# Performance work log

Hardware: AMD Instinct MI355X
Metric: run time of the kernel (lower is better)

## Reference

```python
import jax, jax.numpy as jnp
import numpy as np

S = 41          # seq_len
D_IN = 1280
D_OUT = 1024
HEADS = 4
HC = D_OUT // HEADS
EPS = 1e-5

# ---- static edge construction (faithful to the torch code, incl. duplicate edges) ----

def _local_edges(s, window=1):
    e = []
    for i in range(s):
        for j in range(max(0, i - window), min(s, i + window + 1)):
            if i != j:
                e += [(i, j), (j, i)]
    return np.array(e, dtype=np.int32).T

def _region_edges(s):
    e = []
    step = s // 3
    for st in range(0, s, step):
        blk = range(st, min(st + step, s))
        for i in blk:
            for j in blk:
                if i != j:
                    e += [(i, j), (j, i)]
    return np.array(e, dtype=np.int32).T

def _global_edges(s):
    r, c = np.triu_indices(s, 1)  # torch.combinations: (i, j) with i < j
    return np.stack([r, c]).astype(np.int32)

def _batch_edges(e, b, s):
    off = np.arange(b, dtype=np.int32) * s
    return (e[:, None, :] + off[None, :, None]).reshape(2, -1)

_LOCAL = _local_edges(S)
_REGION = _region_edges(S)
_GLOBAL = _global_edges(S)

# ---- layer primitives ----

def _layernorm(x, g, b):
    mu = x.mean(-1, keepdims=True)
    v = ((x - mu) ** 2).mean(-1, keepdims=True)
    return (x - mu) / jnp.sqrt(v + EPS) * g + b

def _gcn(x, w, b, src, tgt, n):
    # PyG GCNConv: x' = D^-1/2 (A + I) D^-1/2 (x W) + b
    h = x @ w
    sl = jnp.arange(n, dtype=src.dtype)
    s = jnp.concatenate([src, sl]); t = jnp.concatenate([tgt, sl])
    deg = jax.ops.segment_sum(jnp.ones(t.shape, h.dtype), t, n)
    dinv = jnp.where(deg > 0, jax.lax.rsqrt(jnp.maximum(deg, 1.0)), 0.0)
    norm = dinv[s] * dinv[t]
    return jax.ops.segment_sum(h[s] * norm[:, None], t, n) + b

def _gat(x, w, a_src, a_dst, b, src, tgt, n):
    # PyG GATConv (shared lin, self loops, leaky_relu 0.2, softmax over incoming edges)
    h = (x @ w).reshape(n, HEADS, HC)
    sl = jnp.arange(n, dtype=src.dtype)
    s = jnp.concatenate([src, sl]); t = jnp.concatenate([tgt, sl])
    al_s = (h * a_src).sum(-1)  # [n, H]
    al_d = (h * a_dst).sum(-1)
    e = jax.nn.leaky_relu(al_s[s] + al_d[t], 0.2)  # [E, H]
    m = jax.ops.segment_max(e, t, n)
    ex = jnp.exp(e - m[t])
    den = jax.ops.segment_sum(ex, t, n)
    alpha = ex / den[t]
    out = jax.ops.segment_sum(h[s] * alpha[:, :, None], t, n)
    return out.reshape(n, HEADS * HC) + b

def _sage(x, wl, bl, wr, src, tgt, n):
    # PyG SAGEConv: mean-aggregate neighbors, plus root transform
    cnt = jax.ops.segment_sum(jnp.ones(src.shape, x.dtype), tgt, n)
    agg = jax.ops.segment_sum(x[src], tgt, n) / jnp.maximum(cnt, 1.0)[:, None]
    return agg @ wl + bl + x @ wr


def setup_inputs() -> dict:
    key = jax.random.key(0)
    ks = jax.random.split(key, 16)
    sc = 0.02
    f32 = jnp.float32
    inp = {
        'x': jax.random.normal(ks[0], (512, S, D_IN), f32),
        'att_w': jax.random.normal(ks[1], (D_IN, 1), f32) * sc,
        'att_b': jnp.zeros((1,), f32),
        'gcn_w': jax.random.normal(ks[2], (D_IN, D_OUT), f32) * sc,
        'gcn_b': jnp.zeros((D_OUT,), f32),
        'sn_g': jnp.ones((D_OUT,), f32), 'sn_b': jnp.zeros((D_OUT,), f32),
        'gat_w': jax.random.normal(ks[3], (D_IN, D_OUT), f32) * sc,
        'gat_as': jax.random.normal(ks[4], (HEADS, HC), f32) * sc,
        'gat_ad': jax.random.normal(ks[5], (HEADS, HC), f32) * sc,
        'gat_b': jnp.zeros((D_OUT,), f32),
        'mn_g': jnp.ones((D_OUT,), f32), 'mn_b': jnp.zeros((D_OUT,), f32),
        'sage_wl': jax.random.normal(ks[6], (D_IN, D_OUT), f32) * sc,
        'sage_bl': jnp.zeros((D_OUT,), f32),
        'sage_wr': jax.random.normal(ks[7], (D_IN, D_OUT), f32) * sc,
        'fp_w1': jax.random.normal(ks[8], (D_IN, 512), f32) * sc,
        'fp_b1': jnp.zeros((512,), f32),
        'fp_w2': jax.random.normal(ks[9], (512, S), f32) * sc,
        'fp_b2': jnp.zeros((S,), f32),
        'dn_g': jnp.ones((D_OUT,), f32), 'dn_b': jnp.zeros((D_OUT,), f32),
        'gate_w': jax.random.normal(ks[10], (3 * D_OUT, 3), f32) * sc,
        'gate_b': jnp.zeros((3,), f32),
    }
    return inp


def reference(x, att_w, att_b, gcn_w, gcn_b, sn_g, sn_b, gat_w, gat_as, gat_ad, gat_b,
              mn_g, mn_b, sage_wl, sage_bl, sage_wr, fp_w1, fp_b1, fp_w2, fp_b2,
              dn_g, dn_b, gate_w, gate_b):
    B = x.shape[0]
    N = B * S
    le = jnp.asarray(_batch_edges(_LOCAL, B, S))
    re = jnp.asarray(_batch_edges(_REGION, B, S))
    ge = jnp.asarray(_batch_edges(_GLOBAL, B, S))

    xf = x.reshape(N, D_IN)
    # shallow: local gating -> GCN -> LN
    enhanced = xf * jax.nn.sigmoid(xf @ att_w + att_b)
    shallow = _gcn(enhanced, gcn_w, gcn_b, le[0], le[1], N)
    shallow = _layernorm(shallow.reshape(B, S, D_OUT), sn_g, sn_b)
    # medium: GAT over region blocks -> LN
    gat = _gat(xf, gat_w, gat_as[None], gat_ad[None], gat_b, re[0], re[1], N)
    gat = _layernorm(gat.reshape(B, S, D_OUT), mn_g, mn_b)
    # deep: learned propagation mixing, SAGE over global edges -> LN
    pw = jax.nn.softmax(jax.nn.relu(x @ fp_w1 + fp_b1) @ fp_w2 + fp_b2, axis=-1)  # [B,S,S]
    sage_in = jnp.einsum('bij,bjd->bid', pw, x).reshape(N, D_IN)
    sage = _sage(sage_in, sage_wl, sage_bl, sage_wr, ge[0], ge[1], N)
    sage = _layernorm(sage.reshape(B, S, D_OUT), dn_g, dn_b)
    # gated branch mixing
    combined = jnp.concatenate([shallow, gat, sage], axis=-1)
    gates = jax.nn.softmax(combined @ gate_w + gate_b, axis=-1)
    total = gates[..., 0:1] * shallow + gates[..., 1:2] * gat + gates[..., 2:3] * sage
    return (shallow, gat, total)
```

## Files before the change

kernel.cpp:

```cpp
#include <hip/hip_runtime.h>
#include <math.h>

static constexpr int S    = 41;
static constexpr int DIN  = 1280;
static constexpr int DOUT = 1024;
static constexpr int HEADS = 4;
static constexpr int HC   = 256;

typedef __attribute__((ext_vector_type(4))) float f32x4;
typedef __attribute__((ext_vector_type(8))) short short8;

__device__ __forceinline__ ushort f2bf(float f) {
  uint u = __float_as_uint(f);
  uint r = u + 0x7fffu + ((u >> 16) & 1u);
  return (ushort)(r >> 16);
}
__device__ __forceinline__ float bf2f(ushort u) {
  return __uint_as_float(((uint)u) << 16);
}

__device__ __forceinline__ void gload16(const ushort* g, ushort* l) {
  __builtin_amdgcn_global_load_lds((const __attribute__((address_space(1))) void*)g,
                                   (__attribute__((address_space(3))) void*)l, 16, 0, 0);
}


__device__ __forceinline__ float warpReduceSum(float v) {
#pragma unroll
  for (int off = 32; off; off >>= 1) v += __shfl_down(v, off);
  return v;
}

__device__ __forceinline__ void blockReduce6(float* v) {
  __shared__ float red6[6][4];
  int w = threadIdx.x >> 6, lane = threadIdx.x & 63;
#pragma unroll
  for (int r = 0; r < 6; ++r) v[r] = warpReduceSum(v[r]);
  __syncthreads();
  if (lane == 0) {
#pragma unroll
    for (int r = 0; r < 6; ++r) red6[r][w] = v[r];
  }
  __syncthreads();
#pragma unroll
  for (int r = 0; r < 6; ++r)
    v[r] = red6[r][0] + red6[r][1] + red6[r][2] + red6[r][3];
}

__device__ __forceinline__ void blockReduce3v(float* v) {
  __shared__ float red3[3][4];
  int w = threadIdx.x >> 6, lane = threadIdx.x & 63;
#pragma unroll
  for (int r = 0; r < 3; ++r) v[r] = warpReduceSum(v[r]);
  __syncthreads();
  if (lane == 0) {
#pragma unroll
    for (int r = 0; r < 3; ++r) red3[r][w] = v[r];
  }
  __syncthreads();
#pragma unroll
  for (int r = 0; r < 3; ++r)
    v[r] = red3[r][0] + red3[r][1] + red3[r][2] + red3[r][3];
}


__global__ __launch_bounds__(256) void cvtsig_kernel(
    const float4* __restrict__ x, const float* __restrict__ att_w,
    const float* __restrict__ att_b, ushort4* __restrict__ xb, float* __restrict__ sig)
{
  int row  = blockIdx.x * 4 + (threadIdx.x >> 6);
  int lane = threadIdx.x & 63;
  const float4* xr = x + (size_t)row * (DIN / 4);
  const float4* wr = (const float4*)att_w;
  ushort4* xo = xb + (size_t)row * (DIN / 4);
  float acc = 0.f;
#pragma unroll
  for (int k = 0; k < DIN / 4 / 64; ++k) {
    float4 a = xr[lane + k * 64];
    float4 w = wr[lane + k * 64];
    acc += a.x * w.x + a.y * w.y + a.z * w.z + a.w * w.w;
    ushort4 o;
    o.x = f2bf(a.x); o.y = f2bf(a.y); o.z = f2bf(a.z); o.w = f2bf(a.w);
    xo[lane + k * 64] = o;
  }
  acc = warpReduceSum(acc);
  if (lane == 0) sig[row] = 1.f / (1.f + expf(-(acc + att_b[0])));
}


__global__ __launch_bounds__(256) void wcvt_kernel(const float* __restrict__ W,
                                                   ushort* __restrict__ out,
                                                   int K, int N, int ostride, int koff) {
  __shared__ float t[32][33];
  int n0 = blockIdx.x * 32, k0 = blockIdx.y * 32;
  int tx = threadIdx.x & 31, ty = threadIdx.x >> 5;
#pragma unroll
  for (int r = 0; r < 4; ++r) {
    int k = ty + r * 8;
    t[k][tx] = W[(size_t)(k0 + k) * N + n0 + tx];
  }
  __syncthreads();
#pragma unroll
  for (int r = 0; r < 4; ++r) {
    int nn = ty + r * 8;
    out[(size_t)(n0 + nn) * ostride + koff + k0 + tx] = f2bf(t[tx][nn]);
  }
}

__global__ __launch_bounds__(256) void w2cvt_kernel(const float* __restrict__ w2,
                                                    ushort* __restrict__ wpw) {
  int idx = blockIdx.x * 256 + threadIdx.x;
  int n = idx >> 9, k = idx & 511;
  wpw[idx] = (n < S) ? f2bf(w2[(size_t)k * S + n]) : (ushort)0;
}


struct Epi {
  void* dst[5];
  const float* bias[5];
  int nend[5];
  int ld[5];
  int relu[5];
  const float* rs;
};


__global__ __launch_bounds__(512, 1) void gemm8p(
    const ushort* __restrict__ A, const ushort* __restrict__ Bt, int K, int nb, Epi e)
{
  __shared__ __align__(16) ushort As[4 * 8192];
  __shared__ __align__(16) ushort Bs[4 * 8192];

  const int bid = blockIdx.x;
  const int bm  = (bid / nb) * 256;
  const int bn  = (bid % nb) * 256;

  const int tid  = threadIdx.x;
  const int wv   = tid >> 6;
  const int lane = tid & 63;
  const int l16  = lane & 15;
  const int l4   = lane >> 4;
  const int m0   = (wv >> 2) * 128;
  const int n0   = (wv & 3) * 64;

  const int rd0 = wv * 16 + (lane >> 2);
  const int rd1 = 128 + wv * 16 + (lane >> 2);
  const int cs0 = ((lane & 3) - ((rd0 >> 1) & 3)) & 3;
  const int cs1 = ((lane & 3) - ((rd1 >> 1) & 3)) & 3;

  auto stageA = [&](int h, int Tt) {
    int kof = Tt * 64 + (h & 1) * 32;
    gload16(A + (size_t)(bm + rd0) * K + kof + cs0 * 8, &As[h * 8192 + wv * 512]);
    gload16(A + (size_t)(bm + rd1) * K + kof + cs1 * 8, &As[h * 8192 + (8 + wv) * 512]);
  };
  auto stageB = [&](int h, int Tt) {
    int kof = Tt * 64 + (h & 1) * 32;
    gload16(Bt + (size_t)(bn + rd0) * K + kof + cs0 * 8, &Bs[h * 8192 + wv * 512]);
    gload16(Bt + (size_t)(bn + rd1) * K + kof + cs1 * 8, &Bs[h * 8192 + (8 + wv) * 512]);
  };

  const int rchunk = ((l4 + ((l16 >> 1) & 3)) & 3) * 8;

  f32x4 acc[8][4];
#pragma unroll
  for (int i = 0; i < 8; ++i)
#pragma unroll
    for (int j = 0; j < 4; ++j) acc[i][j] = (f32x4)0.f;

  const int NT = K >> 6;

  stageA(0, 0); stageB(0, 0);
  stageA(1, 0); stageB(1, 0);
  stageA(2, 1); stageB(2, 1);

  for (int T = 0; T < NT; ++T) {
    const int db = T & 1;
    const int hA = db * 2;
    const int hB = db * 2 + 1;
    short8 a[4], b[4];

    if (T + 1 < NT) asm volatile("s_waitcnt vmcnt(8)" ::: "memory");
    else            asm volatile("s_waitcnt vmcnt(4)" ::: "memory");
    __builtin_amdgcn_s_barrier();
    asm volatile("" ::: "memory");
    if (T + 1 < NT) stageA((db ^ 1) * 2 + 1, T + 1);
#pragma unroll
    for (int i = 0; i < 4; ++i)
      a[i] = *reinterpret_cast<const short8*>(&As[hA * 8192 + (m0 + i * 16 + l16) * 32 + rchunk]);
#pragma unroll
    for (int j = 0; j < 4; ++j)
      b[j] = *reinterpret_cast<const short8*>(&Bs[hA * 8192 + (n0 + j * 16 + l16) * 32 + rchunk]);
    __builtin_amdgcn_s_setprio(1);
#pragma unroll
    for (int i = 0; i < 4; ++i)
#pragma unroll
      for (int j = 0; j < 4; ++j)
        acc[i][j] = __builtin_amdgcn_mfma_f32_16x16x32_bf16(a[i], b[j], acc[i][j], 0, 0, 0);
    __builtin_amdgcn_s_setprio(0);

    __builtin_amdgcn_s_barrier();
    asm volatile("" ::: "memory");
    if (T + 1 < NT) stageB((db ^ 1) * 2 + 1, T + 1);
#pragma unroll
    for (int i = 0; i < 4; ++i)
      a[i] = *reinterpret_cast<const short8*>(&As[hA * 8192 + (m0 + 64 + i * 16 + l16) * 32 + rchunk]);
    __builtin_amdgcn_s_setprio(1);
#pragma unroll
    for (int i = 0; i < 4; ++i)
#pragma unroll
      for (int j = 0; j < 4; ++j)
        acc[4 + i][j] = __builtin_amdgcn_mfma_f32_16x16x32_bf16(a[i], b[j], acc[4 + i][j], 0, 0, 0);
    __builtin_amdgcn_s_setprio(0);

    if (T + 1 < NT) asm volatile("s_waitcnt vmcnt(8)" ::: "memory");
    else            asm volatile("s_waitcnt vmcnt(0)" ::: "memory");
    __builtin_amdgcn_s_barrier();
    asm volatile("" ::: "memory");
    if (T + 2 < NT) stageA(db * 2, T + 2);
#pragma unroll
    for (int i = 0; i < 4; ++i)
      a[i] = *reinterpret_cast<const short8*>(&As[hB * 8192 + (m0 + i * 16 + l16) * 32 + rchunk]);
#pragma unroll
    for (int j = 0; j < 4; ++j)
      b[j] = *reinterpret_cast<const short8*>(&Bs[hB * 8192 + (n0 + j * 16 + l16) * 32 + rchunk]);
    __builtin_amdgcn_s_setprio(1);
#pragma unroll
    for (int i = 0; i < 4; ++i)
#pragma unroll
      for (int j = 0; j < 4; ++j)
        acc[i][j] = __builtin_amdgcn_mfma_f32_16x16x32_bf16(a[i], b[j], acc[i][j], 0, 0, 0);
    __builtin_amdgcn_s_setprio(0);

    __builtin_amdgcn_s_barrier();
    asm volatile("" ::: "memory");
    if (T + 2 < NT) stageB(db * 2, T + 2);
#pragma unroll
    for (int i = 0; i < 4; ++i)
      a[i] = *reinterpret_cast<const short8*>(&As[hB * 8192 + (m0 + 64 + i * 16 + l16) * 32 + rchunk]);
    __builtin_amdgcn_s_setprio(1);
#pragma unroll
    for (int i = 0; i < 4; ++i)
#pragma unroll
      for (int j = 0; j < 4; ++j)
        acc[4 + i][j] = __builtin_amdgcn_mfma_f32_16x16x32_bf16(a[i], b[j], acc[4 + i][j], 0, 0, 0);
    __builtin_amdgcn_s_setprio(0);
  }

  void* dstv; const float* bias; const float* rs = nullptr; int ldc, cb, relu;
  if (bn < e.nend[0])      { dstv = e.dst[0]; ldc = e.ld[0]; cb = bn;             bias = e.bias[0]; relu = e.relu[0]; rs = e.rs; }
  else if (bn < e.nend[1]) { dstv = e.dst[1]; ldc = e.ld[1]; cb = bn - e.nend[0]; bias = e.bias[1]; relu = e.relu[1]; }
  else if (bn < e.nend[2]) { dstv = e.dst[2]; ldc = e.ld[2]; cb = bn - e.nend[1]; bias = e.bias[2]; relu = e.relu[2]; }
  else if (bn < e.nend[3]) { dstv = e.dst[3]; ldc = e.ld[3]; cb = bn - e.nend[2]; bias = e.bias[3]; relu = e.relu[3]; }
  else                     { dstv = e.dst[4]; ldc = e.ld[4]; cb = bn - e.nend[3]; bias = e.bias[4]; relu = e.relu[4]; }

#pragma unroll
  for (int i = 0; i < 8; ++i) {
    int mbase = bm + m0 + i * 16 + l4 * 4;
    float rsv[4];
#pragma unroll
    for (int r = 0; r < 4; ++r) rsv[r] = rs ? rs[mbase + r] : 1.f;
#pragma unroll
    for (int j = 0; j < 4; ++j) {
      int col = cb + n0 + j * 16 + l16;
      float bv = bias ? bias[col] : 0.f;
#pragma unroll
      for (int r = 0; r < 4; ++r) {
        float t = acc[i][j][r] * rsv[r] + bv;
        if (relu) t = fmaxf(t, 0.f);
        ((ushort*)dstv)[(size_t)(mbase + r) * ldc + col] = f2bf(t);
      }
    }
  }
}


template<bool F32OUT>
__global__ __launch_bounds__(256) void gemm_bf16(
    const ushort* __restrict__ A, const ushort* __restrict__ Bt, int K, int nb, Epi e)
{
  __shared__ __align__(16) ushort As[3][128 * 32];
  __shared__ __align__(16) ushort Bs[3][128 * 32];

  const int bid = blockIdx.x;
  const int bm  = (bid / nb) * 128;
  const int bn  = (bid % nb) * 128;

  const int tid  = threadIdx.x;
  const int w    = tid >> 6;
  const int lane = tid & 63;
  const int l16  = lane & 15;
  const int l4   = lane >> 4;
  const int m0   = (w >> 1) * 64;
  const int n0   = (w & 1) * 64;

  const int rloc = lane >> 2;
  const int cpos = lane & 3;
  const int cdat = (cpos - (rloc >> 1)) & 3;
  const int srow = w * 32 + rloc;
  const int scol = cdat * 8;

  f32x4 acc[4][4];
#pragma unroll
  for (int i = 0; i < 4; ++i)
#pragma unroll
    for (int j = 0; j < 4; ++j) acc[i][j] = (f32x4)0.f;

  const ushort* pA0 = A  + (size_t)(bm + srow) * K + scol;
  const ushort* pA1 = A  + (size_t)(bm + srow + 16) * K + scol;
  const ushort* pB0 = Bt + (size_t)(bn + srow) * K + scol;
  const ushort* pB1 = Bt + (size_t)(bn + srow + 16) * K + scol;

  auto stage = [&](int buf, int kt) {
    gload16(pA0 + kt, &As[buf][w * 1024]);
    gload16(pA1 + kt, &As[buf][w * 1024 + 512]);
    gload16(pB0 + kt, &Bs[buf][w * 1024]);
    gload16(pB1 + kt, &Bs[buf][w * 1024 + 512]);
  };

  const int rchunk = ((l4 + (l16 >> 1)) & 3) * 8;

  const int nsteps = K >> 5;
  stage(0, 0); stage(1, 32); stage(2, 64);

  for (int t = 0; t < nsteps; ++t) {
    if (t == 0)                asm volatile("s_waitcnt vmcnt(8)" ::: "memory");
    else if (t == nsteps - 1)  asm volatile("s_waitcnt vmcnt(0)" ::: "memory");
    else                       asm volatile("s_waitcnt vmcnt(4)" ::: "memory");
    __builtin_amdgcn_s_barrier();
    asm volatile("" ::: "memory");

    if (t >= 1 && t + 2 < nsteps) stage((t + 2) % 3, (t + 2) * 32);

    const int cur = t % 3;
    short8 a[4], b[4];
#pragma unroll
    for (int i = 0; i < 4; ++i)
      a[i] = *reinterpret_cast<const short8*>(&As[cur][(m0 + i * 16 + l16) * 32 + rchunk]);
#pragma unroll
    for (int j = 0; j < 4; ++j)
      b[j] = *reinterpret_cast<const short8*>(&Bs[cur][(n0 + j * 16 + l16) * 32 + rchunk]);
    __builtin_amdgcn_s_setprio(1);
#pragma unroll
    for (int i = 0; i < 4; ++i)
#pragma unroll
      for (int j = 0; j < 4; ++j)
        acc[i][j] = __builtin_amdgcn_mfma_f32_16x16x32_bf16(a[i], b[j], acc[i][j], 0, 0, 0);
    __builtin_amdgcn_s_setprio(0);
  }

  void* dstv; const float* bias; const float* rs = nullptr; int ldc, cb, relu;
  if (bn < e.nend[0])      { dstv = e.dst[0]; ldc = e.ld[0]; cb = bn;             bias = e.bias[0]; relu = e.relu[0]; rs = e.rs; }
  else if (bn < e.nend[1]) { dstv = e.dst[1]; ldc = e.ld[1]; cb = bn - e.nend[0]; bias = e.bias[1]; relu = e.relu[1]; }
  else if (bn < e.nend[2]) { dstv = e.dst[2]; ldc = e.ld[2]; cb = bn - e.nend[1]; bias = e.bias[2]; relu = e.relu[2]; }
  else if (bn < e.nend[3]) { dstv = e.dst[3]; ldc = e.ld[3]; cb = bn - e.nend[2]; bias = e.bias[3]; relu = e.relu[3]; }
  else                     { dstv = e.dst[4]; ldc = e.ld[4]; cb = bn - e.nend[3]; bias = e.bias[4]; relu = e.relu[4]; }

#pragma unroll
  for (int i = 0; i < 4; ++i) {
    int mbase = bm + m0 + i * 16 + l4 * 4;
    float rsv[4];
#pragma unroll
    for (int r = 0; r < 4; ++r) rsv[r] = rs ? rs[mbase + r] : 1.f;
#pragma unroll
    for (int j = 0; j < 4; ++j) {
      int col = cb + n0 + j * 16 + l16;
      float bv = bias ? bias[col] : 0.f;
#pragma unroll
      for (int r = 0; r < 4; ++r) {
        float t = acc[i][j][r] * rsv[r] + bv;
        if (relu) t = fmaxf(t, 0.f);
        if (F32OUT) ((float*)dstv)[(size_t)(mbase + r) * ldc + col] = t;
        else        ((ushort*)dstv)[(size_t)(mbase + r) * ldc + col] = f2bf(t);
      }
    }
  }
}


__global__ __launch_bounds__(256) void pwprep_kernel(
    const float* __restrict__ fp2, const float* __restrict__ fp_b2,
    float* __restrict__ pc)
{
  int b = blockIdx.x;
  int tid = threadIdx.x, wv = tid >> 6, lane = tid & 63;
  __shared__ float pws[S][S];
  for (int i = wv; i < S; i += 4) {
    float v = (lane < S) ? (fp2[(size_t)(b * S + i) * 128 + lane] + fp_b2[lane]) : -1e30f;
    float m = v;
#pragma unroll
    for (int off = 32; off; off >>= 1) m = fmaxf(m, __shfl_xor(m, off));
    float e = (lane < S) ? expf(v - m) : 0.f;
    float sum = e;
#pragma unroll
    for (int off = 32; off; off >>= 1) sum += __shfl_xor(sum, off);
    if (lane < S) {
      float p = e / sum;
      pws[i][lane] = p;
      pc[((size_t)b * S + i) * 128 + lane] = p;
    }
  }
  __syncthreads();
  if (tid < S) {
    float run = 0.f;
    for (int i = 0; i < S; ++i) {
      pc[((size_t)b * S + i) * 128 + 64 + tid] = (i > 0) ? run / (float)i : 0.f;
      run += pws[i][tid];
    }
  }
}


__global__ __launch_bounds__(256) void mixc_kernel(
    const float* __restrict__ pc, const ushort* __restrict__ xr,
    const ushort* __restrict__ xl, const float* __restrict__ sage_bl,
    ushort* __restrict__ hbuf)
{
  int b  = blockIdx.y;
  int d0 = blockIdx.x * 256;
  int tid = threadIdx.x;

  float xrv[S], xlv[S];
  const ushort* xrp = xr + (size_t)(b * S) * DOUT + d0 + tid;
  const ushort* xlp = xl + (size_t)(b * S) * DOUT + d0 + tid;
#pragma unroll
  for (int j = 0; j < S; ++j) {
    xrv[j] = bf2f(xrp[(size_t)j * DOUT]);
    xlv[j] = bf2f(xlp[(size_t)j * DOUT]);
  }
  float bl = sage_bl[d0 + tid];
  ushort* op = hbuf + (size_t)(b * S) * DOUT + d0 + tid;
  const float* pcb = pc + (size_t)(b * S) * 128;
  for (int i = 0; i < S; ++i) {
    const float* row = pcb + (size_t)i * 128;
    float acc = bl;
#pragma unroll
    for (int j = 0; j < S; ++j)
      acc += row[j] * xrv[j] + row[64 + j] * xlv[j];
    op[(size_t)i * DOUT] = f2bf(acc);
  }
}


__device__ __forceinline__ float dinv_local(int j) {
  return rsqrtf((j == 0 || j == S - 1) ? 3.f : 5.f);
}

__global__ __launch_bounds__(256) void tail_fused(
    const ushort* __restrict__ gcnh, const ushort* __restrict__ Cgat,
    const ushort* __restrict__ hbuf,
    const float* __restrict__ gcn_b, const float* __restrict__ sn_g, const float* __restrict__ sn_b,
    const float* __restrict__ gat_as, const float* __restrict__ gat_ad, const float* __restrict__ gat_b,
    const float* __restrict__ mn_g, const float* __restrict__ mn_b,
    const float* __restrict__ dn_g, const float* __restrict__ dn_b,
    const float* __restrict__ gw, const float* __restrict__ gb,
    float* __restrict__ out, int N)
{
  int b  = blockIdx.x >> 2;
  int rb = blockIdx.x & 3;
  int lo = rb * 13;
  int cnt = (rb < 3) ? 13 : 2;
  size_t OUT = (size_t)N * DOUT;
  int tid = threadIdx.x;
  int wv = tid >> 6, lane = tid & 63;
  int d0 = tid * 4;
  int head = tid >> 6;

  __shared__ __align__(16) ushort hs[13][DOUT];
  __shared__ float alpha[13][13][HEADS];
  __shared__ float als_l[13][HEADS], ald_l[13][HEADS];

  for (int r = 0; r < cnt; ++r) {
    const ushort4* src = (const ushort4*)(Cgat + (size_t)(b * S + lo + r) * DOUT);
    ((ushort4*)hs[r])[tid] = src[tid];
  }
  __syncthreads();

  {
    const float4* a4 = (const float4*)(gat_as + wv * HC);
    const float4* d4 = (const float4*)(gat_ad + wv * HC);
    float4 av = a4[lane], dv = d4[lane];
    for (int s = 0; s < cnt; ++s) {
      ushort4 hv4 = ((const ushort4*)&hs[s][wv * HC])[lane];
      float h0 = bf2f(hv4.x), h1 = bf2f(hv4.y), h2 = bf2f(hv4.z), h3 = bf2f(hv4.w);
      float a = h0 * av.x + h1 * av.y + h2 * av.z + h3 * av.w;
      float d = h0 * dv.x + h1 * dv.y + h2 * dv.z + h3 * dv.w;
      a = warpReduceSum(a);
      d = warpReduceSum(d);
      if (lane == 0) { als_l[s][wv] = a; ald_l[s][wv] = d; }
    }
  }
  __syncthreads();

  if (tid < cnt * HEADS) {
    int t = tid >> 2, hd = tid & 3;
    float myald = ald_l[t][hd];
    float m = -1e30f;
    for (int s = 0; s < cnt; ++s) {
      float v = als_l[s][hd] + myald;
      v = (v > 0.f) ? v : 0.2f * v;
      m = fmaxf(m, v);
    }
    float den = 0.f;
    for (int s = 0; s < cnt; ++s) {
      float v = als_l[s][hd] + myald;
      v = (v > 0.f) ? v : 0.2f * v;
      float ev = expf(v - m) * ((s == t) ? 1.f : 2.f);
      alpha[t][s][hd] = ev;
      den += ev;
    }
    float inv = 1.f / den;
    for (int s = 0; s < cnt; ++s) alpha[t][s][hd] *= inv;
  }
  __syncthreads();

  float4 gcnb4 = *(const float4*)(gcn_b + d0);
  float4 sng4  = *(const float4*)(sn_g + d0);
  float4 snb4  = *(const float4*)(sn_b + d0);
  float4 gatb4 = *(const float4*)(gat_b + d0);
  float4 mng4  = *(const float4*)(mn_g + d0);
  float4 mnb4  = *(const float4*)(mn_b + d0);
  float4 dng4  = *(const float4*)(dn_g + d0);
  float4 dnb4  = *(const float4*)(dn_b + d0);
  float gwsh[4][3], gwga[4][3], gwsa[4][3];
#pragma unroll
  for (int q = 0; q < 4; ++q)
#pragma unroll
    for (int c = 0; c < 3; ++c) {
      gwsh[q][c] = gw[(size_t)(d0 + q) * 3 + c];
      gwga[q][c] = gw[(size_t)(DOUT + d0 + q) * 3 + c];
      gwsa[q][c] = gw[(size_t)(2 * DOUT + d0 + q) * 3 + c];
    }

  for (int t = 0; t < cnt; ++t) {
    int i = lo + t;
    size_t n = (size_t)(b * S + i);

    float di = dinv_local(i);
    float wc = di * di;
    float wl = (i > 0)     ? 2.f * di * dinv_local(i - 1) : 0.f;
    float wr = (i < S - 1) ? 2.f * di * dinv_local(i + 1) : 0.f;
    const ushort* hc = gcnh + n * DOUT + d0;
    ushort4 c4  = *(const ushort4*)hc;
    ushort4 lft = (i > 0)     ? *(const ushort4*)(hc - DOUT) : ushort4{0, 0, 0, 0};
    ushort4 rgt = (i < S - 1) ? *(const ushort4*)(hc + DOUT) : ushort4{0, 0, 0, 0};
    const ushort* cp = (const ushort*)&c4;
    const ushort* lp = (const ushort*)&lft;
    const ushort* rp = (const ushort*)&rgt;
    const float* gbp = (const float*)&gcnb4;
    float sh[4];
#pragma unroll
    for (int q = 0; q < 4; ++q)
      sh[q] = wc * bf2f(cp[q]) + wl * bf2f(lp[q]) + wr * bf2f(rp[q]) + gbp[q];

    float ga[4] = {0.f, 0.f, 0.f, 0.f};
    for (int si = 0; si < cnt; ++si) {
      float aj = alpha[t][si][head];
      ushort4 hv = *(const ushort4*)&hs[si][d0];
      ga[0] += aj * bf2f(hv.x);
      ga[1] += aj * bf2f(hv.y);
      ga[2] += aj * bf2f(hv.z);
      ga[3] += aj * bf2f(hv.w);
    }
    const float* gab = (const float*)&gatb4;
#pragma unroll
    for (int q = 0; q < 4; ++q) ga[q] += gab[q];

    ushort4 s4v = *(const ushort4*)(hbuf + n * DOUT + d0);
    const ushort* sp = (const ushort*)&s4v;
    float sa[4];
#pragma unroll
    for (int q = 0; q < 4; ++q) sa[q] = bf2f(sp[q]);

    float red[6] = {0.f, 0.f, 0.f, 0.f, 0.f, 0.f};
#pragma unroll
    for (int q = 0; q < 4; ++q) {
      red[0] += sh[q]; red[1] += sh[q] * sh[q];
      red[2] += ga[q]; red[3] += ga[q] * ga[q];
      red[4] += sa[q]; red[5] += sa[q] * sa[q];
    }
    blockReduce6(red);
    float mu0 = red[0] * (1.f / DOUT), r0 = rsqrtf(red[1] * (1.f / DOUT) - mu0 * mu0 + 1e-5f);
    float mu1 = red[2] * (1.f / DOUT), r1 = rsqrtf(red[3] * (1.f / DOUT) - mu1 * mu1 + 1e-5f);
    float mu2 = red[4] * (1.f / DOUT), r2 = rsqrtf(red[5] * (1.f / DOUT) - mu2 * mu2 + 1e-5f);

    const float* sngp = (const float*)&sng4; const float* snbp = (const float*)&snb4;
    const float* mngp = (const float*)&mng4; const float* mnbp = (const float*)&mnb4;
    const float* dngp = (const float*)&dng4; const float* dnbp = (const float*)&dnb4;
    float shn[4], gan[4], san[4];
#pragma unroll
    for (int q = 0; q < 4; ++q) {
      shn[q] = (sh[q] - mu0) * r0 * sngp[q] + snbp[q];
      gan[q] = (ga[q] - mu1) * r1 * mngp[q] + mnbp[q];
      san[q] = (sa[q] - mu2) * r2 * dngp[q] + dnbp[q];
    }

    float p[3] = {0.f, 0.f, 0.f};
#pragma unroll
    for (int q = 0; q < 4; ++q) {
#pragma unroll
      for (int c = 0; c < 3; ++c)
        p[c] += shn[q] * gwsh[q][c] + gan[q] * gwga[q][c] + san[q] * gwsa[q][c];
    }
    blockReduce3v(p);
    float l0 = p[0] + gb[0], l1 = p[1] + gb[1], l2 = p[2] + gb[2];
    float m = fmaxf(l0, fmaxf(l1, l2));
    float e0 = expf(l0 - m), e1 = expf(l1 - m), e2 = expf(l2 - m);
    float inv = 1.f / (e0 + e1 + e2);
    float g0 = e0 * inv, g1 = e1 * inv, g2 = e2 * inv;

    float4 o0, o1, o2;
    float* o0p = (float*)&o0; float* o1p = (float*)&o1; float* o2p = (float*)&o2;
#pragma unroll
    for (int q = 0; q < 4; ++q) {
      o0p[q] = shn[q];
      o1p[q] = gan[q];
      o2p[q] = g0 * shn[q] + g1 * gan[q] + g2 * san[q];
    }
    *(float4*)(out + n * DOUT + d0)           = o0;
    *(float4*)(out + OUT + n * DOUT + d0)     = o1;
    *(float4*)(out + 2 * OUT + n * DOUT + d0) = o2;
  }
}


extern "C" void kernel_launch(void* const* d_in, const int* in_sizes, int n_in,
                              void* d_out, int out_size, void* d_ws, size_t ws_size,
                              hipStream_t stream) {
  const float* x       = (const float*)d_in[0];
  const float* att_w   = (const float*)d_in[1];
  const float* att_b   = (const float*)d_in[2];
  const float* gcn_w   = (const float*)d_in[3];
  const float* gcn_b   = (const float*)d_in[4];
  const float* sn_g    = (const float*)d_in[5];
  const float* sn_b    = (const float*)d_in[6];
  const float* gat_w   = (const float*)d_in[7];
  const float* gat_as  = (const float*)d_in[8];
  const float* gat_ad  = (const float*)d_in[9];
  const float* gat_b   = (const float*)d_in[10];
  const float* mn_g    = (const float*)d_in[11];
  const float* mn_b    = (const float*)d_in[12];
  const float* sage_wl = (const float*)d_in[13];
  const float* sage_bl = (const float*)d_in[14];
  const float* sage_wr = (const float*)d_in[15];
  const float* fp_w1   = (const float*)d_in[16];
  const float* fp_b1   = (const float*)d_in[17];
  const float* fp_w2   = (const float*)d_in[18];
  const float* fp_b2   = (const float*)d_in[19];
  const float* dn_g    = (const float*)d_in[20];
  const float* dn_b    = (const float*)d_in[21];
  const float* gate_w  = (const float*)d_in[22];
  const float* gate_b  = (const float*)d_in[23];

  const int B = in_sizes[0] / (S * DIN);
  const int N = B * S;
  const int MB  = N / 128;
  const int MB2 = N / 256;
  const int NMEGA = 4608;
  float* out = (float*)d_out;

  char* ws = (char*)d_ws;
  size_t off = 0;
  auto alloc = [&](size_t bytes) { size_t p = off; off += (bytes + 255) & ~(size_t)255; return p; };
  ushort* xb   = (ushort*)(ws + alloc((size_t)N * DIN * 2));
  ushort* Bt   = (ushort*)(ws + alloc((size_t)NMEGA * DIN * 2));
  ushort* wpw  = (ushort*)(ws + alloc((size_t)128 * 512 * 2));
  ushort* gcnh = (ushort*)(ws + alloc((size_t)N * DOUT * 2));
  ushort* Cgat = (ushort*)(ws + alloc((size_t)N * DOUT * 2));
  ushort* xr   = (ushort*)(ws + alloc((size_t)N * DOUT * 2));
  ushort* xl   = (ushort*)(ws + alloc((size_t)N * DOUT * 2));
  ushort* hbuf = (ushort*)(ws + alloc((size_t)N * DOUT * 2));
  float*  fp2  = (float*)(ws + alloc((size_t)N * 128 * 4));
  float*  pc   = (float*)(ws + alloc((size_t)N * 128 * 4));
  float*  sig  = (float*)(ws + alloc((size_t)N * 4));
  ushort* fp1  = hbuf;

  dim3 blk(256);

  cvtsig_kernel<<<N / 4, blk, 0, stream>>>((const float4*)x, att_w, att_b, (ushort4*)xb, sig);
  wcvt_kernel<<<dim3(DOUT / 32, DIN / 32), blk, 0, stream>>>(gcn_w, Bt, DIN, DOUT, DIN, 0);
  wcvt_kernel<<<dim3(DOUT / 32, DIN / 32), blk, 0, stream>>>(gat_w, Bt + (size_t)1024 * DIN, DIN, DOUT, DIN, 0);
  wcvt_kernel<<<dim3(512 / 32, DIN / 32), blk, 0, stream>>>(fp_w1, Bt + (size_t)2048 * DIN, DIN, 512, DIN, 0);
  wcvt_kernel<<<dim3(DOUT / 32, DIN / 32), blk, 0, stream>>>(sage_wr, Bt + (size_t)2560 * DIN, DIN, DOUT, DIN, 0);
  wcvt_kernel<<<dim3(DOUT / 32, DIN / 32), blk, 0, stream>>>(sage_wl, Bt + (size_t)3584 * DIN, DIN, DOUT, DIN, 0);
  w2cvt_kernel<<<dim3(128 * 512 / 256), blk, 0, stream>>>(fp_w2, wpw);

  Epi e1;
  e1.dst[0] = gcnh; e1.dst[1] = Cgat; e1.dst[2] = fp1; e1.dst[3] = xr; e1.dst[4] = xl;
  e1.bias[0] = nullptr; e1.bias[1] = nullptr; e1.bias[2] = fp_b1; e1.bias[3] = nullptr; e1.bias[4] = nullptr;
  e1.nend[0] = 1024; e1.nend[1] = 2048; e1.nend[2] = 2560; e1.nend[3] = 3584; e1.nend[4] = 4608;
  e1.ld[0] = DOUT; e1.ld[1] = DOUT; e1.ld[2] = 512; e1.ld[3] = DOUT; e1.ld[4] = DOUT;
  e1.relu[0] = 0; e1.relu[1] = 0; e1.relu[2] = 1; e1.relu[3] = 0; e1.relu[4] = 0;
  e1.rs = sig;
  gemm8p<<<dim3(MB2 * (NMEGA / 256)), dim3(512), 0, stream>>>(xb, Bt, DIN, NMEGA / 256, e1);

  Epi epw;
  epw.dst[0] = fp2; epw.dst[1] = nullptr; epw.dst[2] = nullptr; epw.dst[3] = nullptr; epw.dst[4] = nullptr;
  epw.bias[0] = nullptr; epw.bias[1] = nullptr; epw.bias[2] = nullptr; epw.bias[3] = nullptr; epw.bias[4] = nullptr;
  epw.nend[0] = 1 << 30; epw.nend[1] = 1 << 30; epw.nend[2] = 1 << 30; epw.nend[3] = 1 << 30; epw.nend[4] = 1 << 30;
  epw.ld[0] = 128; epw.ld[1] = 128; epw.ld[2] = 128; epw.ld[3] = 128; epw.ld[4] = 128;
  epw.relu[0] = 0; epw.relu[1] = 0; epw.relu[2] = 0; epw.relu[3] = 0; epw.relu[4] = 0;
  epw.rs = nullptr;
  gemm_bf16<true><<<dim3(MB), blk, 0, stream>>>(fp1, wpw, 512, 1, epw);

  pwprep_kernel<<<B, blk, 0, stream>>>(fp2, fp_b2, pc);
  mixc_kernel<<<dim3(DOUT / 256, B), blk, 0, stream>>>(pc, xr, xl, sage_bl, hbuf);

  tail_fused<<<B * 4, blk, 0, stream>>>(gcnh, Cgat, hbuf,
                                        gcn_b, sn_g, sn_b,
                                        gat_as, gat_ad, gat_b,
                                        mn_g, mn_b, dn_g, dn_b,
                                        gate_w, gate_b, out, N);
}
```

Before: 693.2 us.

## Remap GEMM workgroups per XCD and restructure pipeline barriers around MFMA clusters

Blocks of the 256x256 GEMM are remapped so that consecutive tiles land on the same XCD, which should improve L2 reuse of shared A/B rows. The main loop is reorganised into a ping-pong style schedule: LDS fragment reads and async global-to-LDS stage issues happen before a barrier, then each MFMA cluster runs between barriers, and waitcnts move next to the stage issues. This aims to overlap memory issue with compute more tightly, at the cost of more barriers per iteration.

```diff
diff --git a/kernel.cpp b/kernel.cpp
--- a/kernel.cpp
+++ b/kernel.cpp
@@ -23,6 +23,8 @@
   __builtin_amdgcn_global_load_lds((const __attribute__((address_space(1))) void*)g,
                                    (__attribute__((address_space(3))) void*)l, 16, 0, 0);
 }
+
+#define FENCE() asm volatile("" ::: "memory")
 
 
 __device__ __forceinline__ float warpReduceSum(float v) {
@@ -131,9 +133,16 @@
   __shared__ __align__(16) ushort As[4 * 8192];
   __shared__ __align__(16) ushort Bs[4 * 8192];
 
-  const int bid = blockIdx.x;
-  const int bm  = (bid / nb) * 256;
-  const int bn  = (bid % nb) * 256;
+  int wg;
+  {
+    const int nwg = gridDim.x;
+    const int bid = blockIdx.x;
+    const int xcd = bid & 7, lin = bid >> 3;
+    const int q = nwg >> 3, r = nwg & 7;
+    wg = (xcd < r) ? (xcd * (q + 1) + lin) : (r * (q + 1) + (xcd - r) * q + lin);
+  }
+  const int bm = (wg / nb) * 256;
+  const int bn = (wg % nb) * 256;
 
   const int tid  = threadIdx.x;
   const int wv   = tid >> 6;
@@ -172,6 +181,9 @@
   stageA(0, 0); stageB(0, 0);
   stageA(1, 0); stageB(1, 0);
   stageA(2, 1); stageB(2, 1);
+  asm volatile("s_waitcnt vmcnt(8)" ::: "memory");
+  __builtin_amdgcn_s_barrier();
+  FENCE();
 
   for (int T = 0; T < NT; ++T) {
     const int db = T & 1;
@@ -179,17 +191,14 @@
     const int hB = db * 2 + 1;
     short8 a[4], b[4];
 
-    if (T + 1 < NT) asm volatile("s_waitcnt vmcnt(8)" ::: "memory");
-    else            asm volatile("s_waitcnt vmcnt(4)" ::: "memory");
-    __builtin_amdgcn_s_barrier();
-    asm volatile("" ::: "memory");
-    if (T + 1 < NT) stageA((db ^ 1) * 2 + 1, T + 1);
 #pragma unroll
     for (int i = 0; i < 4; ++i)
       a[i] = *reinterpret_cast<const short8*>(&As[hA * 8192 + (m0 + i * 16 + l16) * 32 + rchunk]);
 #pragma unroll
     for (int j = 0; j < 4; ++j)
       b[j] = *reinterpret_cast<const short8*>(&Bs[hA * 8192 + (n0 + j * 16 + l16) * 32 + rchunk]);
+    if (T + 1 < NT) stageA((db ^ 1) * 2 + 1, T + 1);
+    FENCE(); __builtin_amdgcn_s_barrier(); FENCE();
     __builtin_amdgcn_s_setprio(1);
 #pragma unroll
     for (int i = 0; i < 4; ++i)
@@ -197,13 +206,18 @@
       for (int j = 0; j < 4; ++j)
         acc[i][j] = __builtin_amdgcn_mfma_f32_16x16x32_bf16(a[i], b[j], acc[i][j], 0, 0, 0);
     __builtin_amdgcn_s_setprio(0);
-
-    __builtin_amdgcn_s_barrier();
-    asm volatile("" ::: "memory");
-    if (T + 1 < NT) stageB((db ^ 1) * 2 + 1, T + 1);
+    FENCE(); __builtin_amdgcn_s_barrier(); FENCE();
+
 #pragma unroll
     for (int i = 0; i < 4; ++i)
       a[i] = *reinterpret_cast<const short8*>(&As[hA * 8192 + (m0 + 64 + i * 16 + l16) * 32 + rchunk]);
+    if (T + 1 < NT) {
+      stageB((db ^ 1) * 2 + 1, T + 1);
+      asm volatile("s_waitcnt vmcnt(8)" ::: "memory");
+    } else {
+      asm volatile("s_waitcnt vmcnt(0)" ::: "memory");
+    }
+    FENCE(); __builtin_amdgcn_s_barrier(); FENCE();
     __builtin_amdgcn_s_setprio(1);
 #pragma unroll
     for (int i = 0; i < 4; ++i)
@@ -211,18 +225,16 @@
       for (int j = 0; j < 4; ++j)
         acc[4 + i][j] = __builtin_amdgcn_mfma_f32_16x16x32_bf16(a[i], b[j], acc[4 + i][j], 0, 0, 0);
     __builtin_amdgcn_s_setprio(0);
-
-    if (T + 1 < NT) asm volatile("s_waitcnt vmcnt(8)" ::: "memory");
-    else            asm volatile("s_waitcnt vmcnt(0)" ::: "memory");
-    __builtin_amdgcn_s_barrier();
-    asm volatile("" ::: "memory");
-    if (T + 2 < NT) stageA(db * 2, T + 2);
+    FENCE(); __builtin_amdgcn_s_barrier(); FENCE();
+
 #pragma unroll
     for (int i = 0; i < 4; ++i)
       a[i] = *reinterpret_cast<const short8*>(&As[hB * 8192 + (m0 + i * 16 + l16) * 32 + rchunk]);
 #pragma unroll
     for (int j = 0; j < 4; ++j)
       b[j] = *reinterpret_cast<const short8*>(&Bs[hB * 8192 + (n0 + j * 16 + l16) * 32 + rchunk]);
+    if (T + 2 < NT) stageA(hA, T + 2);
+    FENCE(); __builtin_amdgcn_s_barrier(); FENCE();
     __builtin_amdgcn_s_setprio(1);
 #pragma unroll
     for (int i = 0; i < 4; ++i)
@@ -230,13 +242,18 @@
       for (int j = 0; j < 4; ++j)
         acc[i][j] = __builtin_amdgcn_mfma_f32_16x16x32_bf16(a[i], b[j], acc[i][j], 0, 0, 0);
     __builtin_amdgcn_s_setprio(0);
-
-    __builtin_amdgcn_s_barrier();
-    asm volatile("" ::: "memory");
-    if (T + 2 < NT) stageB(db * 2, T + 2);
+    FENCE(); __builtin_amdgcn_s_barrier(); FENCE();
+
 #pragma unroll
     for (int i = 0; i < 4; ++i)
       a[i] = *reinterpret_cast<const short8*>(&As[hB * 8192 + (m0 + 64 + i * 16 + l16) * 32 + rchunk]);
+    if (T + 2 < NT) {
+      stageB(hA, T + 2);
+      asm volatile("s_waitcnt vmcnt(8)" ::: "memory");
+    } else if (T + 1 < NT) {
+      asm volatile("s_waitcnt vmcnt(4)" ::: "memory");
+    }
+    FENCE(); __builtin_amdgcn_s_barrier(); FENCE();
     __builtin_amdgcn_s_setprio(1);
 #pragma unroll
     for (int i = 0; i < 4; ++i)
@@ -244,6 +261,7 @@
       for (int j = 0; j < 4; ++j)
         acc[4 + i][j] = __builtin_amdgcn_mfma_f32_16x16x32_bf16(a[i], b[j], acc[4 + i][j], 0, 0, 0);
     __builtin_amdgcn_s_setprio(0);
+    FENCE(); __builtin_amdgcn_s_barrier(); FENCE();
   }
 
   void* dstv; const float* bias; const float* rs = nullptr; int ldc, cb, relu;
@@ -327,7 +345,7 @@
     else if (t == nsteps - 1)  asm volatile("s_waitcnt vmcnt(0)" ::: "memory");
     else                       asm volatile("s_waitcnt vmcnt(4)" ::: "memory");
     __builtin_amdgcn_s_barrier();
-    asm volatile("" ::: "memory");
+    FENCE();
 
     if (t >= 1 && t + 2 < nsteps) stage((t + 2) % 3, (t + 2) * 32);
 
```

Measured after the change: 652.1 us. 5.9% less time.
